# Performance work log

Hardware: AMD Instinct MI355X
Metric: run time of the kernel (lower is better)

## Reference

```python
import jax, jax.numpy as jnp
import numpy as np

D_MODEL = 1024
NUM_HEADS = 16
HEAD_DIM = D_MODEL // NUM_HEADS
WINDOW = 64
BATCH = 2
SEQ = 2048


def setup_inputs() -> dict:
    key = jax.random.key(0)
    ks = jax.random.split(key, 5)
    s = 1.0 / np.sqrt(D_MODEL)  # torch Linear-ish init scale
    x = jax.random.normal(ks[0], (BATCH, SEQ, D_MODEL), dtype=jnp.float32)
    Wq = jax.random.normal(ks[1], (D_MODEL, D_MODEL), dtype=jnp.float32) * s
    Wk = jax.random.normal(ks[2], (D_MODEL, D_MODEL), dtype=jnp.float32) * s
    Wv = jax.random.normal(ks[3], (D_MODEL, D_MODEL), dtype=jnp.float32) * s
    Wo = jax.random.normal(ks[4], (D_MODEL, D_MODEL), dtype=jnp.float32) * s
    z = jnp.zeros((D_MODEL,), dtype=jnp.float32)
    return {"x": x, "Wq": Wq, "bq": z, "Wk": Wk, "bk": z, "Wv": Wv, "bv": z,
            "Wo": Wo, "bo": z}


def reference(x, Wq, bq, Wk, bk, Wv, bv, Wo, bo):
    B, S, D = x.shape
    H, Hd = NUM_HEADS, HEAD_DIM
    # QKV projections; weights stored as [in, out] so y = x @ W + b
    q = (x @ Wq + bq).reshape(B, S, H, Hd).transpose(0, 2, 1, 3)  # bhsd
    k = (x @ Wk + bk).reshape(B, S, H, Hd).transpose(0, 2, 1, 3)
    v = (x @ Wv + bv).reshape(B, S, H, Hd).transpose(0, 2, 1, 3)
    scores = jnp.einsum('bhqd,bhkd->bhqk', q, k) / jnp.sqrt(jnp.float32(Hd))
    # static local-window band mask: attend only where |i - j| <= window_size
    idx = jnp.arange(S)
    dist = jnp.abs(idx[None, :] - idx[:, None])  # [S, S]
    scores = jnp.where(dist[None, None] > WINDOW, -jnp.inf, scores)
    attn = jax.nn.softmax(scores, axis=-1)
    out = jnp.einsum('bhqk,bhkd->bhqd', attn, v)
    out = out.transpose(0, 2, 1, 3).reshape(B, S, D)
    return out @ Wo + bo
```

## Files before the change

### kernel.cpp

```cpp
#include <hip/hip_runtime.h>
#include <cstdint>
#include <cstddef>

typedef __bf16 bf16x8 __attribute__((ext_vector_type(8)));
typedef float  f32x4  __attribute__((ext_vector_type(4)));

__device__ __forceinline__ unsigned short f2bf(float f) {
    union { __bf16 b; unsigned short u; } cv; cv.b = (__bf16)f; return cv.u;
}
__device__ __forceinline__ int iclamp(int v, int lo, int hi) {
    return v < lo ? lo : (v > hi ? hi : v);
}

__device__ __forceinline__ void gload16(const void* gsrc, void* ldsdst) {
    __builtin_amdgcn_global_load_lds(
        (const __attribute__((address_space(1))) unsigned int*)(uintptr_t)gsrc,
        (__attribute__((address_space(3))) unsigned int*)(uintptr_t)ldsdst,
        16, 0, 0);
}

#define MFMA16(a, b, c) __builtin_amdgcn_mfma_f32_16x16x32_bf16((a), (b), (c), 0, 0, 0)

__global__ __launch_bounds__(256) void castx(const float* __restrict__ x,
                                             unsigned short* __restrict__ xb) {
    size_t i = ((size_t)blockIdx.x * 256 + threadIdx.x) * 8;
    float4 a = *(const float4*)(x + i);
    float4 b = *(const float4*)(x + i + 4);
    union { unsigned short u[8]; uint4 q; } pk;
    pk.u[0] = f2bf(a.x); pk.u[1] = f2bf(a.y); pk.u[2] = f2bf(a.z); pk.u[3] = f2bf(a.w);
    pk.u[4] = f2bf(b.x); pk.u[5] = f2bf(b.y); pk.u[6] = f2bf(b.z); pk.u[7] = f2bf(b.w);
    *(uint4*)(xb + i) = pk.q;
}

__global__ __launch_bounds__(256) void wt_kernel(const float* __restrict__ Wq,
                                                 const float* __restrict__ Wk,
                                                 const float* __restrict__ Wv,
                                                 const float* __restrict__ Wo,
                                                 unsigned short* __restrict__ Wt) {
    __shared__ float tile[64][65];
    const int z = blockIdx.z;
    const float* W = (z == 0) ? Wq : (z == 1) ? Wk : (z == 2) ? Wv : Wo;
    const int n0 = blockIdx.x * 64, k0 = blockIdx.y * 64;
    const int tid = threadIdx.x;
    const int tr = tid >> 4, tc = (tid & 15) * 4;
#pragma unroll
    for (int i = 0; i < 4; ++i) {
        int r = tr + i * 16;
        float4 v = *(const float4*)(W + (size_t)(k0 + r) * 1024 + n0 + tc);
        tile[r][tc + 0] = v.x; tile[r][tc + 1] = v.y;
        tile[r][tc + 2] = v.z; tile[r][tc + 3] = v.w;
    }
    __syncthreads();
    const int n = tid & 63, kc = (tid >> 6) * 16;
    union { unsigned short u[16]; uint4 q[2]; } pk;
#pragma unroll
    for (int c = 0; c < 16; ++c) pk.u[c] = f2bf(tile[kc + c][n]);
    uint4* dst = (uint4*)(Wt + (size_t)z * 1048576 + (size_t)(n0 + n) * 1024 + k0 + kc);
    dst[0] = pk.q[0]; dst[1] = pk.q[1];
}

__global__ __launch_bounds__(256) void bias_cat_k(const float* __restrict__ bq,
                                                  const float* __restrict__ bk,
                                                  const float* __restrict__ bv,
                                                  float* __restrict__ bc) {
    int i = blockIdx.x * 256 + threadIdx.x;
    bc[i] = (i < 1024) ? bq[i] : (i < 2048) ? bk[i - 1024] : bv[i - 2048];
}

__device__ __forceinline__ void gemm_mainloop(const unsigned short* __restrict__ A,
                                              const unsigned short* __restrict__ Bt,
                                              int K, int m0, int n0,
                                              unsigned short* Asm, unsigned short* Bsm,
                                              f32x4 acc[4][4]) {
    const int tid = threadIdx.x;
    const int wave = tid >> 6, lane = tid & 63;
    const int lq = lane & 15, quad = lane >> 4;

    const int rstage = wave * 16 + (lane >> 2);
    const int sw8 = ((lane & 3) ^ quad) * 8;
    const unsigned short* gA0 = A + (size_t)(m0 + rstage) * K + sw8;
    const unsigned short* gA1 = A + (size_t)(m0 + 64 + rstage) * K + sw8;
    const unsigned short* gB0 = Bt + (size_t)(n0 + rstage) * K + sw8;
    const unsigned short* gB1 = Bt + (size_t)(n0 + 64 + rstage) * K + sw8;
    unsigned short* lA0 = Asm + (wave * 16) * 32;
    unsigned short* lA1 = Asm + (64 + wave * 16) * 32;
    unsigned short* lB0 = Bsm + (wave * 16) * 32;
    unsigned short* lB1 = Bsm + (64 + wave * 16) * 32;

    int offA[4], offB[4];
    const int pos8 = (quad ^ (lq >> 2)) * 8;
#pragma unroll
    for (int i = 0; i < 4; ++i) {
        offA[i] = ((wave >> 1) * 64 + i * 16 + lq) * 32 + pos8;
        offB[i] = ((wave & 1) * 64 + i * 16 + lq) * 32 + pos8;
    }

    for (int kt = 0; kt < K; kt += 32) {
        gload16(gA0 + kt, lA0);
        gload16(gA1 + kt, lA1);
        gload16(gB0 + kt, lB0);
        gload16(gB1 + kt, lB1);
        __syncthreads();
        bf16x8 af[4], bfr[4];
#pragma unroll
        for (int i = 0; i < 4; ++i) af[i] = *(const bf16x8*)(Asm + offA[i]);
#pragma unroll
        for (int j = 0; j < 4; ++j) bfr[j] = *(const bf16x8*)(Bsm + offB[j]);
#pragma unroll
        for (int i = 0; i < 4; ++i)
#pragma unroll
            for (int j = 0; j < 4; ++j)
                acc[i][j] = MFMA16(af[i], bfr[j], acc[i][j]);
        __syncthreads();
    }
}

__global__ __launch_bounds__(256, 2) void gemm_qkv(const unsigned short* __restrict__ xb,
                                                   const unsigned short* __restrict__ Wt,
                                                   const float* __restrict__ bcat,
                                                   unsigned short* __restrict__ Qb,
                                                   unsigned short* __restrict__ Kb,
                                                   unsigned short* __restrict__ Vt) {
    __shared__ __align__(16) unsigned short Asm[128 * 32];
    __shared__ __align__(16) unsigned short Bsm[128 * 32];
    f32x4 acc[4][4];
#pragma unroll
    for (int i = 0; i < 4; ++i)
#pragma unroll
        for (int j = 0; j < 4; ++j) acc[i][j] = f32x4{0.f, 0.f, 0.f, 0.f};
    const int m0 = blockIdx.y * 128, n0 = blockIdx.x * 128;
    gemm_mainloop(xb, Wt, 1024, m0, n0, Asm, Bsm, acc);

    const int tid = threadIdx.x, wave = tid >> 6, lane = tid & 63;
    const int lq = lane & 15, quad = lane >> 4;
#pragma unroll
    for (int i = 0; i < 4; ++i) {
#pragma unroll
        for (int j = 0; j < 4; ++j) {
            const int n = n0 + (wave & 1) * 64 + j * 16 + lq;
            const int p = n >> 10, c = n & 1023, h = c >> 6, d = c & 63;
            const float bi = bcat[n];
#pragma unroll
            for (int r = 0; r < 4; ++r) {
                const int m = m0 + (wave >> 1) * 64 + i * 16 + quad * 4 + r;
                const int b = m >> 11, s = m & 2047;
                const unsigned short v = f2bf(acc[i][j][r] + bi);
                if (p == 0)
                    Qb[(size_t)((b * 16 + h) * 2048 + s) * 64 + d] = v;
                else if (p == 1)
                    Kb[(size_t)((b * 16 + h) * 2048 + s) * 64 + d] = v;
                else
                    Vt[(size_t)((b * 16 + h) * 64 + d) * 2048 + s] = v;
            }
        }
    }
}

__global__ __launch_bounds__(256, 4) void attn_k(const unsigned short* __restrict__ Qb,
                                                 const unsigned short* __restrict__ Kb,
                                                 const unsigned short* __restrict__ Vt,
                                                 unsigned short* __restrict__ AO) {
    __shared__ __align__(16) unsigned short P[4][16 * 168];
    const int tid = threadIdx.x, wave = tid >> 6, lane = tid & 63;
    const int lq = lane & 15, quad = lane >> 4;
    const int b = blockIdx.z, h = blockIdx.y;
    const int q0 = blockIdx.x * 64 + wave * 16;
    const unsigned short* Qh = Qb + (size_t)((b * 16 + h) * 2048) * 64;
    const unsigned short* Kh = Kb + (size_t)((b * 16 + h) * 2048) * 64;
    const unsigned short* Vh = Vt + (size_t)((b * 16 + h) * 64) * 2048;
    unsigned short* pw = P[wave];

    {
        unsigned int* zp = (unsigned int*)(pw + (lane >> 2) * 168 + 144 + (lane & 3) * 4);
        zp[0] = 0u; zp[1] = 0u;
    }

    const bf16x8 qa0 = *(const bf16x8*)(Qh + (size_t)(q0 + lq) * 64 + quad * 8);
    const bf16x8 qa1 = *(const bf16x8*)(Qh + (size_t)(q0 + lq) * 64 + 32 + quad * 8);

    float sc[9][4];
    float mr[4] = {-3e38f, -3e38f, -3e38f, -3e38f};
#pragma unroll
    for (int t = 0; t < 9; ++t) {
        const int kb = q0 - 64 + t * 16;
        const int krow = kb + lq;
        const int krc = iclamp(krow, 0, 2047);
        const unsigned short* kp = Kh + (size_t)krc * 64 + quad * 8;
        const bf16x8 kf0 = *(const bf16x8*)kp;
        const bf16x8 kf1 = *(const bf16x8*)(kp + 32);
        f32x4 cacc = f32x4{0.f, 0.f, 0.f, 0.f};
        cacc = MFMA16(qa0, kf0, cacc);
        cacc = MFMA16(qa1, kf1, cacc);
#pragma unroll
        for (int r = 0; r < 4; ++r) {
            const int q = q0 + quad * 4 + r;
            const int dj = q - krow;
            const bool ok = (krow >= 0) && (krow < 2048) && (dj <= 64) && (dj >= -64);
            const float s = ok ? cacc[r] * 0.125f : -3e38f;
            sc[t][r] = s;
            mr[r] = fmaxf(mr[r], s);
        }
    }
#pragma unroll
    for (int r = 0; r < 4; ++r) {
#pragma unroll
        for (int off = 1; off < 16; off <<= 1)
            mr[r] = fmaxf(mr[r], __shfl_xor(mr[r], off));
    }
    float ls[4] = {0.f, 0.f, 0.f, 0.f};
#pragma unroll
    for (int t = 0; t < 9; ++t)
#pragma unroll
        for (int r = 0; r < 4; ++r) {
            const float p = __expf(sc[t][r] - mr[r]);
            sc[t][r] = p;
            ls[r] += p;
        }
#pragma unroll
    for (int r = 0; r < 4; ++r) {
#pragma unroll
        for (int off = 1; off < 16; off <<= 1)
            ls[r] += __shfl_xor(ls[r], off);
    }
    float rinv[4];
#pragma unroll
    for (int r = 0; r < 4; ++r) rinv[r] = 1.f / ls[r];

#pragma unroll
    for (int t = 0; t < 9; ++t)
#pragma unroll
        for (int r = 0; r < 4; ++r)
            pw[(quad * 4 + r) * 168 + t * 16 + lq] = f2bf(sc[t][r]);

    f32x4 oa[4];
#pragma unroll
    for (int dt = 0; dt < 4; ++dt) oa[dt] = f32x4{0.f, 0.f, 0.f, 0.f};
#pragma unroll
    for (int ks = 0; ks < 5; ++ks) {
        const bf16x8 pf = *(const bf16x8*)(pw + lq * 168 + ks * 32 + quad * 8);
        int s0 = q0 - 64 + ks * 32 + quad * 8;
        s0 = iclamp(s0, 0, 2040);
#pragma unroll
        for (int dt = 0; dt < 4; ++dt) {
            const bf16x8 vf = *(const bf16x8*)(Vh + (size_t)(dt * 16 + lq) * 2048 + s0);
            oa[dt] = MFMA16(pf, vf, oa[dt]);
        }
    }
#pragma unroll
    for (int dt = 0; dt < 4; ++dt)
#pragma unroll
        for (int r = 0; r < 4; ++r) {
            const int q = q0 + quad * 4 + r;
            AO[(size_t)(b * 2048 + q) * 1024 + h * 64 + dt * 16 + lq] =
                f2bf(oa[dt][r] * rinv[r]);
        }
}

__global__ __launch_bounds__(256, 2) void gemm_out(const unsigned short* __restrict__ AO,
                                                   const unsigned short* __restrict__ Wot,
                                                   const float* __restrict__ bo,
                                                   float* __restrict__ out) {
    __shared__ __align__(16) unsigned short Asm[128 * 32];
    __shared__ __align__(16) unsigned short Bsm[128 * 32];
    f32x4 acc[4][4];
#pragma unroll
    for (int i = 0; i < 4; ++i)
#pragma unroll
        for (int j = 0; j < 4; ++j) acc[i][j] = f32x4{0.f, 0.f, 0.f, 0.f};
    const int m0 = blockIdx.y * 128, n0 = blockIdx.x * 128;
    gemm_mainloop(AO, Wot, 1024, m0, n0, Asm, Bsm, acc);

    const int tid = threadIdx.x, wave = tid >> 6, lane = tid & 63;
    const int lq = lane & 15, quad = lane >> 4;
#pragma unroll
    for (int i = 0; i < 4; ++i) {
#pragma unroll
        for (int j = 0; j < 4; ++j) {
            const int n = n0 + (wave & 1) * 64 + j * 16 + lq;
            const float bi = bo[n];
#pragma unroll
            for (int r = 0; r < 4; ++r) {
                const int m = m0 + (wave >> 1) * 64 + i * 16 + quad * 4 + r;
                out[(size_t)m * 1024 + n] = acc[i][j][r] + bi;
            }
        }
    }
}

extern "C" void kernel_launch(void* const* d_in, const int* in_sizes, int n_in,
                              void* d_out, int out_size, void* d_ws, size_t ws_size,
                              hipStream_t stream) {
    const float* x  = (const float*)d_in[0];
    const float* Wq = (const float*)d_in[1];
    const float* bq = (const float*)d_in[2];
    const float* Wk = (const float*)d_in[3];
    const float* bk = (const float*)d_in[4];
    const float* Wv = (const float*)d_in[5];
    const float* bv = (const float*)d_in[6];
    const float* Wo = (const float*)d_in[7];
    const float* bo = (const float*)d_in[8];
    float* out = (float*)d_out;

    unsigned short* us = (unsigned short*)d_ws;
    const size_t MEG = 1048576;
    unsigned short* xb = us;
    unsigned short* Wt = us + 4 * MEG;
    unsigned short* Qb = us + 8 * MEG;
    unsigned short* Kb = us + 12 * MEG;
    unsigned short* Vt = us + 16 * MEG;
    unsigned short* AO = us + 20 * MEG;
    float* bcat = (float*)(us + 24 * MEG);

    castx<<<2048, 256, 0, stream>>>(x, xb);
    wt_kernel<<<dim3(16, 16, 4), 256, 0, stream>>>(Wq, Wk, Wv, Wo, Wt);
    bias_cat_k<<<12, 256, 0, stream>>>(bq, bk, bv, bcat);
    gemm_qkv<<<dim3(24, 32), 256, 0, stream>>>(xb, Wt, bcat, Qb, Kb, Vt);
    attn_k<<<dim3(32, 16, 2), 256, 0, stream>>>(Qb, Kb, Vt, AO);
    gemm_out<<<dim3(8, 32), 256, 0, stream>>>(AO, Wt + 3 * MEG, bo, out);
}
```

Measured before the change: 184.5 us.

## Stage QKV epilogue through LDS for coalesced stores; shrink out-proj tile

The QKV GEMM epilogue now writes each wave's 16x64 output sub-tile into reused shared memory, then issues 16-byte stores: row-contiguous for Q/K and transposed along the sequence for V. This replaces the scattered 2-byte stores, which were especially bad for the transposed V layout. The output projection GEMM uses a 128x64 tile with its own mainloop, doubling the block count to 512 to improve occupancy across CUs. The cost is extra LDS round trips in the epilogue and lower per-block reuse in gemm_out.

```diff
diff --git a/kernel.cpp b/kernel.cpp
--- a/kernel.cpp
+++ b/kernel.cpp
@@ -121,8 +121,9 @@
                                                    unsigned short* __restrict__ Qb,
                                                    unsigned short* __restrict__ Kb,
                                                    unsigned short* __restrict__ Vt) {
-    __shared__ __align__(16) unsigned short Asm[128 * 32];
-    __shared__ __align__(16) unsigned short Bsm[128 * 32];
+    __shared__ __align__(16) unsigned short smem[8192];
+    unsigned short* Asm = smem;
+    unsigned short* Bsm = smem + 4096;
     f32x4 acc[4][4];
 #pragma unroll
     for (int i = 0; i < 4; ++i)
@@ -133,24 +134,44 @@
 
     const int tid = threadIdx.x, wave = tid >> 6, lane = tid & 63;
     const int lq = lane & 15, quad = lane >> 4;
+    const int p = n0 >> 10;
+    const int nloc = (wave & 1) * 64;
+    const int c64 = (n0 + nloc) & 1023;
+    const int h = c64 >> 6;
+    const int b = m0 >> 11;
+    const int mw = m0 + (wave >> 1) * 64;
+    const int mloc = mw & 2047;
+    unsigned short* sw = smem + wave * 1152;
+
+    float bi[4];
+#pragma unroll
+    for (int j = 0; j < 4; ++j) bi[j] = bcat[n0 + nloc + j * 16 + lq];
+
+    unsigned short* qkbase = (p == 0) ? Qb : Kb;
+
 #pragma unroll
     for (int i = 0; i < 4; ++i) {
 #pragma unroll
-        for (int j = 0; j < 4; ++j) {
-            const int n = n0 + (wave & 1) * 64 + j * 16 + lq;
-            const int p = n >> 10, c = n & 1023, h = c >> 6, d = c & 63;
-            const float bi = bcat[n];
-#pragma unroll
-            for (int r = 0; r < 4; ++r) {
-                const int m = m0 + (wave >> 1) * 64 + i * 16 + quad * 4 + r;
-                const int b = m >> 11, s = m & 2047;
-                const unsigned short v = f2bf(acc[i][j][r] + bi);
-                if (p == 0)
-                    Qb[(size_t)((b * 16 + h) * 2048 + s) * 64 + d] = v;
-                else if (p == 1)
-                    Kb[(size_t)((b * 16 + h) * 2048 + s) * 64 + d] = v;
-                else
-                    Vt[(size_t)((b * 16 + h) * 64 + d) * 2048 + s] = v;
+        for (int j = 0; j < 4; ++j)
+#pragma unroll
+            for (int r = 0; r < 4; ++r)
+                sw[(quad * 4 + r) * 72 + j * 16 + lq] = f2bf(acc[i][j][r] + bi[j]);
+        if (p < 2) {
+            const int row = lane >> 2, c0 = (lane & 3) * 8;
+            uint4 v0 = *(const uint4*)(sw + row * 72 + c0);
+            uint4 v1 = *(const uint4*)(sw + row * 72 + c0 + 32);
+            const int s = mloc + i * 16 + row;
+            unsigned short* dp = qkbase + ((size_t)((b * 16 + h) * 2048 + s)) * 64;
+            *(uint4*)(dp + c0) = v0;
+            *(uint4*)(dp + c0 + 32) = v1;
+        } else {
+#pragma unroll
+            for (int th = 0; th < 2; ++th) {
+                union { unsigned short u[8]; uint4 q; } pk;
+#pragma unroll
+                for (int t = 0; t < 8; ++t) pk.u[t] = sw[(th * 8 + t) * 72 + lane];
+                const int sbase = mloc + i * 16 + th * 8;
+                *(uint4*)(Vt + ((size_t)((b * 16 + h) * 64 + lane)) * 2048 + sbase) = pk.q;
             }
         }
     }
@@ -261,22 +282,58 @@
                                                    const float* __restrict__ bo,
                                                    float* __restrict__ out) {
     __shared__ __align__(16) unsigned short Asm[128 * 32];
-    __shared__ __align__(16) unsigned short Bsm[128 * 32];
-    f32x4 acc[4][4];
-#pragma unroll
-    for (int i = 0; i < 4; ++i)
-#pragma unroll
-        for (int j = 0; j < 4; ++j) acc[i][j] = f32x4{0.f, 0.f, 0.f, 0.f};
-    const int m0 = blockIdx.y * 128, n0 = blockIdx.x * 128;
-    gemm_mainloop(AO, Wot, 1024, m0, n0, Asm, Bsm, acc);
-
+    __shared__ __align__(16) unsigned short Bsm[64 * 32];
     const int tid = threadIdx.x, wave = tid >> 6, lane = tid & 63;
     const int lq = lane & 15, quad = lane >> 4;
+    const int m0 = blockIdx.y * 128, n0 = blockIdx.x * 64;
+
+    f32x4 acc[4][2];
+#pragma unroll
+    for (int i = 0; i < 4; ++i)
+#pragma unroll
+        for (int j = 0; j < 2; ++j) acc[i][j] = f32x4{0.f, 0.f, 0.f, 0.f};
+
+    const int rstage = wave * 16 + (lane >> 2);
+    const int sw8 = ((lane & 3) ^ quad) * 8;
+    const unsigned short* gA0 = AO + (size_t)(m0 + rstage) * 1024 + sw8;
+    const unsigned short* gA1 = AO + (size_t)(m0 + 64 + rstage) * 1024 + sw8;
+    const unsigned short* gB0 = Wot + (size_t)(n0 + rstage) * 1024 + sw8;
+    unsigned short* lA0 = Asm + (wave * 16) * 32;
+    unsigned short* lA1 = Asm + (64 + wave * 16) * 32;
+    unsigned short* lB0 = Bsm + (wave * 16) * 32;
+
+    int offA[4], offB[2];
+    const int pos8 = (quad ^ (lq >> 2)) * 8;
+#pragma unroll
+    for (int i = 0; i < 4; ++i)
+        offA[i] = ((wave >> 1) * 64 + i * 16 + lq) * 32 + pos8;
+#pragma unroll
+    for (int j = 0; j < 2; ++j)
+        offB[j] = ((wave & 1) * 32 + j * 16 + lq) * 32 + pos8;
+
+    for (int kt = 0; kt < 1024; kt += 32) {
+        gload16(gA0 + kt, lA0);
+        gload16(gA1 + kt, lA1);
+        gload16(gB0 + kt, lB0);
+        __syncthreads();
+        bf16x8 af[4], bfr[2];
+#pragma unroll
+        for (int i = 0; i < 4; ++i) af[i] = *(const bf16x8*)(Asm + offA[i]);
+#pragma unroll
+        for (int j = 0; j < 2; ++j) bfr[j] = *(const bf16x8*)(Bsm + offB[j]);
+#pragma unroll
+        for (int i = 0; i < 4; ++i)
+#pragma unroll
+            for (int j = 0; j < 2; ++j)
+                acc[i][j] = MFMA16(af[i], bfr[j], acc[i][j]);
+        __syncthreads();
+    }
+
 #pragma unroll
     for (int i = 0; i < 4; ++i) {
 #pragma unroll
-        for (int j = 0; j < 4; ++j) {
-            const int n = n0 + (wave & 1) * 64 + j * 16 + lq;
+        for (int j = 0; j < 2; ++j) {
+            const int n = n0 + (wave & 1) * 32 + j * 16 + lq;
             const float bi = bo[n];
 #pragma unroll
             for (int r = 0; r < 4; ++r) {
@@ -316,5 +373,5 @@
     bias_cat_k<<<12, 256, 0, stream>>>(bq, bk, bv, bcat);
     gemm_qkv<<<dim3(24, 32), 256, 0, stream>>>(xb, Wt, bcat, Qb, Kb, Vt);
     attn_k<<<dim3(32, 16, 2), 256, 0, stream>>>(Qb, Kb, Vt, AO);
-    gemm_out<<<dim3(8, 32), 256, 0, stream>>>(AO, Wt + 3 * MEG, bo, out);
-}
+    gemm_out<<<dim3(16, 32), 256, 0, stream>>>(AO, Wt + 3 * MEG, bo, out);
+}
```

New measurement: 174.4 us. -5.5%, faster.
